# Performance work log

Measured on AMD Instinct MI355X. Metric: run time of the kernel, lower is better.

Reference implementation:

```python
import jax, jax.numpy as jnp
import numpy as np

C = 512
IC = C // 2
BN_EPS = 1e-5

def conv1x1(x, w, b):
    # x: (b,c,h,w), w: (o,c), b: (o,)
    return jnp.einsum('bchw,oc->bohw', x, w) + b[None, :, None, None]

def setup_inputs() -> dict:
    key = jax.random.key(0)
    ks = jax.random.split(key, 9)
    b, h, w = 8, 48, 48
    x = jax.random.normal(ks[0], (b, C, h, w), dtype=jnp.float32)
    s = 1.0 / np.sqrt(C)
    g_w = jax.random.normal(ks[1], (IC, C), dtype=jnp.float32) * s
    g_b = jnp.zeros((IC,), jnp.float32)
    theta_w = jax.random.normal(ks[2], (IC, C), dtype=jnp.float32) * s
    theta_b = jnp.zeros((IC,), jnp.float32)
    phi_w = jax.random.normal(ks[3], (IC, C), dtype=jnp.float32) * s
    phi_b = jnp.zeros((IC,), jnp.float32)
    w_w = jax.random.normal(ks[4], (C, IC), dtype=jnp.float32) * (1.0 / np.sqrt(IC))
    w_b = jnp.zeros((C,), jnp.float32)
    # BatchNorm affine params: initialized to 0 per nn.init.constant_ in source
    bn_gamma = jnp.zeros((C,), jnp.float32)
    bn_beta = jnp.zeros((C,), jnp.float32)
    return {"x": x, "g_w": g_w, "g_b": g_b, "theta_w": theta_w, "theta_b": theta_b,
            "phi_w": phi_w, "phi_b": phi_b, "w_w": w_w, "w_b": w_b,
            "bn_gamma": bn_gamma, "bn_beta": bn_beta}

def reference(x, g_w, g_b, theta_w, theta_b, phi_w, phi_b, w_w, w_b, bn_gamma, bn_beta):
    b, c, h, w = x.shape
    hw = h * w
    g_x = conv1x1(x, g_w, g_b).reshape(b, IC, hw).transpose(0, 2, 1)      # (b,hw,ic)
    theta_x = conv1x1(x, theta_w, theta_b).reshape(b, IC, hw).transpose(0, 2, 1)  # (b,hw,ic)
    phi_x = conv1x1(x, phi_w, phi_b).reshape(b, IC, hw)                    # (b,ic,hw)
    f = jnp.einsum('bqc,bck->bqk', theta_x, phi_x)                         # (b,hw,hw), unscaled
    f_div_C = jax.nn.softmax(f, axis=-1)
    y = jnp.einsum('bqk,bkc->bqc', f_div_C, g_x)                           # (b,hw,ic)
    y = y.transpose(0, 2, 1).reshape(b, IC, h, w)
    wy = conv1x1(y, w_w, w_b)                                              # (b,c,h,w)
    # BatchNorm2d in training mode: batch statistics over (b,h,w)
    mean = jnp.mean(wy, axis=(0, 2, 3), keepdims=True)
    var = jnp.var(wy, axis=(0, 2, 3), keepdims=True)
    wy_bn = (wy - mean) / jnp.sqrt(var + BN_EPS)
    wy_bn = wy_bn * bn_gamma[None, :, None, None] + bn_beta[None, :, None, None]
    return wy_bn + x
```

## Files before the change

kernel.cpp:

```cpp
#include <hip/hip_runtime.h>
#include <hip/hip_bf16.h>
#include <stdint.h>

constexpr int Bn  = 8;
constexpr int Cc  = 512;
constexpr int ICc = 256;
constexpr int HWc = 48 * 48;
constexpr float BN_EPS = 1e-5f;

typedef unsigned short u16;
typedef __attribute__((ext_vector_type(8))) short short8;
typedef __attribute__((ext_vector_type(4))) float f32x4;

__device__ __forceinline__ u16 f2bf(float f) {
    uint32_t u = __builtin_bit_cast(uint32_t, f);
    u += 0x7fffu + ((u >> 16) & 1u);
    return (u16)(u >> 16);
}
__device__ __forceinline__ void load_lds16(const void* g, void* l) {
    __builtin_amdgcn_global_load_lds(
        (const __attribute__((address_space(1))) void*)(uintptr_t)g,
        (__attribute__((address_space(3))) void*)(uintptr_t)l, 16, 0, 0);
}

__global__ __launch_bounds__(256)
void cast_front(const float* __restrict__ th_w, const float* __restrict__ ph_w,
                const float* __restrict__ g_w, const float* __restrict__ th_b,
                const float* __restrict__ ph_b, u16* __restrict__ wcat,
                float* __restrict__ bias_thph) {
    int idx = blockIdx.x * 256 + threadIdx.x;
    if (idx < 98304) {
        const float4* src;
        if (idx < 32768)       src = (const float4*)th_w + idx;
        else if (idx < 65536)  src = (const float4*)ph_w + (idx - 32768);
        else                   src = (const float4*)g_w  + (idx - 65536);
        float4 v = *src;
        ushort4 o;
        o.x = f2bf(v.x); o.y = f2bf(v.y); o.z = f2bf(v.z); o.w = f2bf(v.w);
        ((ushort4*)wcat)[idx] = o;
    } else if (idx < 98816) {
        int i = idx - 98304;
        bias_thph[i] = (i < 256) ? th_b[i] : ph_b[i - 256];
    }
}

__global__ __launch_bounds__(256)
void cast_w(const float* __restrict__ a, u16* __restrict__ out) {
    int idx = blockIdx.x * 256 + threadIdx.x;
    float4 v = ((const float4*)a)[idx];
    ushort4 o;
    o.x = f2bf(v.x); o.y = f2bf(v.y); o.z = f2bf(v.z); o.w = f2bf(v.w);
    ((ushort4*)out)[idx] = o;
}

__global__ __launch_bounds__(256)
void transpose_cast_x(const float* __restrict__ x, u16* __restrict__ xt) {
    __shared__ float t[64][33];
    const int b = blockIdx.z;
    const int p0 = blockIdx.x * 32;
    const int c0 = blockIdx.y * 64;
    const int tx = threadIdx.x & 31, ty = threadIdx.x >> 5;
    const float* xb = x + (size_t)b * Cc * HWc;
#pragma unroll
    for (int r = 0; r < 8; ++r)
        t[r * 8 + ty][tx] = xb[(size_t)(c0 + r * 8 + ty) * HWc + p0 + tx];
    __syncthreads();
    u16* xtb = xt + (size_t)b * HWc * Cc;
    const int cc = (threadIdx.x & 31) * 2, pp = threadIdx.x >> 5;
#pragma unroll
    for (int r = 0; r < 4; ++r) {
        int p = r * 8 + pp;
        ushort2 v;
        v.x = f2bf(t[cc][p]);
        v.y = f2bf(t[cc + 1][p]);
        *(ushort2*)&xtb[(size_t)(p0 + p) * Cc + c0 + cc] = v;
    }
}

template <int TM, int STORE, bool STATS>
__global__ __launch_bounds__(256, 2)
void mfma_gemm(const u16* __restrict__ A, const u16* __restrict__ B,
               void* __restrict__ Cout, const float* __restrict__ bias,
               int bias_mode, int K, int ldA, int ldB, int ldC,
               size_t sA, size_t sB, size_t sC,
               float* __restrict__ s0g, float* __restrict__ s1g) {
    constexpr int MI = TM / 32;
    __shared__ __align__(16) u16 As[TM * 32];
    __shared__ __align__(16) u16 Bs[128 * 32];
    const int bz = blockIdx.z;
    const int m0 = blockIdx.y * TM, n0 = blockIdx.x * 128;
    const u16* Ab = A + (size_t)bz * sA + (size_t)m0 * ldA;
    const u16* Bb = B + (size_t)bz * sB + (size_t)n0 * ldB;
    const int tid = threadIdx.x, lane = tid & 63, w = tid >> 6;
    const int wm = (w & 1) * (TM / 2);
    const int wn = (w >> 1) * 64;
    const int quad = lane >> 4, m16 = lane & 15;

    f32x4 acc[MI][4];
#pragma unroll
    for (int i = 0; i < MI; ++i)
#pragma unroll
        for (int j = 0; j < 4; ++j) acc[i][j] = (f32x4){0.f, 0.f, 0.f, 0.f};

    const int L0 = 2 * w * 64 + lane, L1 = L0 + 64;
    const int br0 = L0 >> 2, bc0 = (L0 & 3) * 8;
    const int br1 = L1 >> 2, bc1 = (L1 & 3) * 8;
    const int ar0 = (TM == 128) ? br0 : (tid >> 2);
    const int ac0 = (TM == 128) ? bc0 : (tid & 3) * 8;

    for (int k0 = 0; k0 < K; k0 += 32) {
        if (TM == 128) {
            load_lds16(Ab + (size_t)ar0 * ldA + k0 + ac0, &As[2 * w * 512]);
            load_lds16(Ab + (size_t)br1 * ldA + k0 + bc1, &As[(2 * w + 1) * 512]);
        } else {
            load_lds16(Ab + (size_t)ar0 * ldA + k0 + ac0, &As[w * 512]);
        }
        load_lds16(Bb + (size_t)br0 * ldB + k0 + bc0, &Bs[2 * w * 512]);
        load_lds16(Bb + (size_t)br1 * ldB + k0 + bc1, &Bs[(2 * w + 1) * 512]);
        __syncthreads();

        short8 af[MI], bfv[4];
#pragma unroll
        for (int i = 0; i < MI; ++i)
            af[i] = *(const short8*)&As[(wm + i * 16 + m16) * 32 + quad * 8];
#pragma unroll
        for (int j = 0; j < 4; ++j)
            bfv[j] = *(const short8*)&Bs[(wn + j * 16 + m16) * 32 + quad * 8];
#pragma unroll
        for (int i = 0; i < MI; ++i)
#pragma unroll
            for (int j = 0; j < 4; ++j)
                acc[i][j] = __builtin_amdgcn_mfma_f32_16x16x32_bf16(
                    af[i], bfv[j], acc[i][j], 0, 0, 0);
        __syncthreads();
    }

    if (bias_mode) {
#pragma unroll
        for (int i = 0; i < MI; ++i)
#pragma unroll
            for (int j = 0; j < 4; ++j)
#pragma unroll
                for (int r = 0; r < 4; ++r)
                    acc[i][j][r] += (bias_mode == 2)
                        ? bias[m0 + wm + i * 16 + quad * 4 + r]
                        : bias[n0 + wn + j * 16 + m16];
    }

    if (STORE == 0) {
        u16* C = (u16*)Cout + (size_t)bz * sC;
#pragma unroll
        for (int i = 0; i < MI; ++i) {
            int m = m0 + wm + i * 16 + quad * 4;
#pragma unroll
            for (int j = 0; j < 4; ++j) {
                int n = n0 + wn + j * 16 + m16;
#pragma unroll
                for (int r = 0; r < 4; ++r)
                    C[(size_t)(m + r) * ldC + n] = f2bf(acc[i][j][r]);
            }
        }
    } else {
        float* C = (float*)Cout + (size_t)bz * sC;
#pragma unroll
        for (int i = 0; i < MI; ++i) {
            int m = m0 + wm + i * 16 + quad * 4;
#pragma unroll
            for (int j = 0; j < 4; ++j) {
                int n = n0 + wn + j * 16 + m16;
#pragma unroll
                for (int r = 0; r < 4; ++r)
                    C[(size_t)(m + r) * ldC + n] = acc[i][j][r];
            }
        }
    }

    if (STATS) {
#pragma unroll
        for (int i = 0; i < MI; ++i) {
#pragma unroll
            for (int r = 0; r < 4; ++r) {
                float v0 = 0.f, v1 = 0.f;
#pragma unroll
                for (int j = 0; j < 4; ++j) {
                    float v = acc[i][j][r];
                    v0 += v;
                    v1 = fmaf(v, v, v1);
                }
#pragma unroll
                for (int off = 8; off; off >>= 1) {
                    v0 += __shfl_down(v0, off, 16);
                    v1 += __shfl_down(v1, off, 16);
                }
                if (m16 == 0) {
                    int m = m0 + wm + i * 16 + quad * 4 + r;
                    atomicAdd(&s0g[m], v0);
                    atomicAdd(&s1g[m], v1);
                }
            }
        }
    }
}

__global__ __launch_bounds__(256, 2)
void flash_attn(const u16* __restrict__ thph, const u16* __restrict__ g,
                u16* __restrict__ y) {
    __shared__ __align__(16) u16 smem[25088];
    const int bz = blockIdx.y;
    const int q0 = blockIdx.x * 64;
    const u16* Qb = thph + (size_t)bz * HWc * 512 + (size_t)q0 * 512;
    const u16* Kb = thph + (size_t)bz * HWc * 512 + 256;
    const u16* Vb = g + (size_t)bz * ICc * HWc;
    const int tid = threadIdx.x, lane = tid & 63, w = tid >> 6;
    const int quad = lane >> 4, m16 = lane & 15;
    const int wm = w * 16;

#pragma unroll
    for (int t = 0; t < 8; ++t) {
        int L = (w * 8 + t) * 64 + lane;
        int row = L >> 5, col = (L & 31) * 8;
        load_lds16(Qb + (size_t)row * 512 + col, &smem[8192 + (w * 8 + t) * 512]);
    }
    __syncthreads();
    short8 qf[8];
#pragma unroll
    for (int c = 0; c < 8; ++c)
        qf[c] = *(const short8*)&smem[8192 + (wm + m16) * 256 + c * 32 + quad * 8];
    __syncthreads();

    f32x4 O[16];
#pragma unroll
    for (int i = 0; i < 16; ++i) O[i] = (f32x4){0.f, 0.f, 0.f, 0.f};
    float mrow[4] = {-1e30f, -1e30f, -1e30f, -1e30f};
    float lrow[4] = {0.f, 0.f, 0.f, 0.f};

    for (int kt = 0; kt < 18; ++kt) {
        const u16* Kt = Kb + (size_t)kt * 128 * 512;
        f32x4 Sa[8];
#pragma unroll
        for (int j = 0; j < 8; ++j) Sa[j] = (f32x4){0.f, 0.f, 0.f, 0.f};

#pragma unroll
        for (int kc = 0; kc < 4; ++kc) {
#pragma unroll
            for (int h = 0; h < 2; ++h) {
                int cdim = (kc * 2 + h) * 32;
#pragma unroll
                for (int t = 0; t < 2; ++t) {
                    int L = (w * 2 + t) * 64 + lane;
                    int row = L >> 2, col = (L & 3) * 8;
                    load_lds16(Kt + (size_t)row * 512 + cdim + col,
                               &smem[h * 4096 + (w * 2 + t) * 512]);
                }
            }
            __syncthreads();
#pragma unroll
            for (int h = 0; h < 2; ++h)
#pragma unroll
                for (int j = 0; j < 8; ++j) {
                    short8 kf = *(const short8*)
                        &smem[h * 4096 + (j * 16 + m16) * 32 + quad * 8];
                    Sa[j] = __builtin_amdgcn_mfma_f32_16x16x32_bf16(
                        qf[kc * 2 + h], kf, Sa[j], 0, 0, 0);
                }
            __syncthreads();
        }

        float alpha[4];
#pragma unroll
        for (int r = 0; r < 4; ++r) {
            float tm = Sa[0][r];
#pragma unroll
            for (int j = 1; j < 8; ++j) tm = fmaxf(tm, Sa[j][r]);
#pragma unroll
            for (int off = 1; off < 16; off <<= 1)
                tm = fmaxf(tm, __shfl_xor(tm, off, 16));
            float nm = fmaxf(mrow[r], tm);
            alpha[r] = __expf(mrow[r] - nm);
            mrow[r] = nm;
            float ps = 0.f;
#pragma unroll
            for (int j = 0; j < 8; ++j) {
                float p = __expf(Sa[j][r] - nm);
                Sa[j][r] = p;
                ps += p;
            }
#pragma unroll
            for (int off = 1; off < 16; off <<= 1)
                ps += __shfl_xor(ps, off, 16);
            lrow[r] = lrow[r] * alpha[r] + ps;
        }
#pragma unroll
        for (int j2 = 0; j2 < 16; ++j2)
#pragma unroll
            for (int r = 0; r < 4; ++r) O[j2][r] *= alpha[r];

        u16* Pw = &smem[16384 + w * 2176];
#pragma unroll
        for (int j = 0; j < 8; ++j)
#pragma unroll
            for (int r = 0; r < 4; ++r)
                Pw[(quad * 4 + r) * 136 + j * 16 + m16] = f2bf(Sa[j][r]);
        short8 pf[4];
#pragma unroll
        for (int c2 = 0; c2 < 4; ++c2)
            pf[c2] = *(const short8*)&Pw[m16 * 136 + c2 * 32 + quad * 8];

#pragma unroll
        for (int c2 = 0; c2 < 4; ++c2) {
            int keyc = kt * 128 + c2 * 32;
#pragma unroll
            for (int t = 0; t < 4; ++t) {
                int L = (w * 4 + t) * 64 + lane;
                int row = L >> 2, col = (L & 3) * 8;
                load_lds16(Vb + (size_t)row * HWc + keyc + col,
                           &smem[8192 + (w * 4 + t) * 512]);
            }
            __syncthreads();
#pragma unroll
            for (int j2 = 0; j2 < 16; ++j2) {
                short8 vf = *(const short8*)
                    &smem[8192 + (j2 * 16 + m16) * 32 + quad * 8];
                O[j2] = __builtin_amdgcn_mfma_f32_16x16x32_bf16(
                    pf[c2], vf, O[j2], 0, 0, 0);
            }
            __syncthreads();
        }
    }

    float rinv[4];
#pragma unroll
    for (int r = 0; r < 4; ++r) rinv[r] = 1.0f / lrow[r];
    u16* yb = y + ((size_t)bz * HWc + q0 + wm) * ICc;
#pragma unroll
    for (int j2 = 0; j2 < 16; ++j2)
#pragma unroll
        for (int r = 0; r < 4; ++r)
            yb[(size_t)(quad * 4 + r) * ICc + j2 * 16 + m16] =
                f2bf(O[j2][r] * rinv[r]);
}

__global__ __launch_bounds__(256)
void bn_apply(const float* __restrict__ wy, const float* __restrict__ x,
              const float* __restrict__ s0, const float* __restrict__ s1,
              const float* __restrict__ gamma, const float* __restrict__ beta,
              float* __restrict__ out) {
    const size_t i4 = (size_t)blockIdx.x * 256 + threadIdx.x;
    const size_t base = i4 * 4;
    const int o = (int)((base / HWc) % Cc);
    const float N = (float)(Bn * HWc);
    const float mean = s0[o] / N;
    const float var  = s1[o] / N - mean * mean;
    const float rstd = rsqrtf(var + BN_EPS);
    const float ga = gamma[o];
    const float be = beta[o];
    const float4 w4 = ((const float4*)wy)[i4];
    const float4 x4 = ((const float4*)x)[i4];
    float4 r;
    r.x = (w4.x - mean) * rstd * ga + be + x4.x;
    r.y = (w4.y - mean) * rstd * ga + be + x4.y;
    r.z = (w4.z - mean) * rstd * ga + be + x4.z;
    r.w = (w4.w - mean) * rstd * ga + be + x4.w;
    ((float4*)out)[i4] = r;
}

extern "C" void kernel_launch(void* const* d_in, const int* in_sizes, int n_in,
                              void* d_out, int out_size, void* d_ws, size_t ws_size,
                              hipStream_t stream) {
    const float* x     = (const float*)d_in[0];
    const float* g_w   = (const float*)d_in[1];
    const float* g_b   = (const float*)d_in[2];
    const float* th_w  = (const float*)d_in[3];
    const float* th_b  = (const float*)d_in[4];
    const float* ph_w  = (const float*)d_in[5];
    const float* ph_b  = (const float*)d_in[6];
    const float* w_w   = (const float*)d_in[7];
    const float* w_b   = (const float*)d_in[8];
    const float* gamma = (const float*)d_in[9];
    const float* beta  = (const float*)d_in[10];

    char* base = (char*)d_ws;
    u16* thph = (u16*)base;
    u16* g    = (u16*)(base + 18874368);
    u16* xt   = (u16*)(base + 28311552);
    u16* wcat = (u16*)(base + 47185920);
    float* bias_thph = (float*)(base + 47972352);
    u16* wbf2 = (u16*)(base + 47974400);
    float* stats = (float*)(base + 48236544);
    u16* y    = (u16*)(base + 48240640);
    float* wy = (float*)(base + 57677824);

    dim3 blk(256);
    const u16* thphw = wcat;
    const u16* gwb   = wcat + 262144;

    cast_front<<<dim3(386), blk, 0, stream>>>(th_w, ph_w, g_w, th_b, ph_b,
                                              wcat, bias_thph);
    cast_w<<<dim3(128), blk, 0, stream>>>(w_w, wbf2);
    hipMemsetAsync(stats, 0, 2 * Cc * sizeof(float), stream);
    transpose_cast_x<<<dim3(HWc / 32, Cc / 64, Bn), blk, 0, stream>>>(x, xt);

    mfma_gemm<128, 0, false><<<dim3(4, 18, Bn), blk, 0, stream>>>(
        xt, thphw, thph, bias_thph, 1, Cc, Cc, Cc, 512,
        (size_t)HWc * Cc, 0, (size_t)HWc * 512, nullptr, nullptr);

    mfma_gemm<64, 0, false><<<dim3(18, 4, Bn), blk, 0, stream>>>(
        gwb, xt, g, g_b, 2, Cc, Cc, Cc, HWc,
        0, (size_t)HWc * Cc, (size_t)ICc * HWc, nullptr, nullptr);

    flash_attn<<<dim3(HWc / 64, Bn), blk, 0, stream>>>(thph, g, y);

    mfma_gemm<128, 1, true><<<dim3(18, 4, Bn), blk, 0, stream>>>(
        wbf2, y, wy, w_b, 2, ICc, ICc, ICc, HWc,
        0, (size_t)HWc * ICc, (size_t)Cc * HWc, stats, stats + Cc);

    bn_apply<<<dim3((Bn * Cc * HWc) / 4 / 256), blk, 0, stream>>>(
        wy, x, stats, stats + Cc, gamma, beta, (float*)d_out);
}
```

Measured before the change: 361.1 us.

## Split flash attention over key range with partial outputs and combine kernel

Result: slower. 391.0 us (+8.3%).

```diff
diff --git a/kernel.cpp b/kernel.cpp
--- a/kernel.cpp
+++ b/kernel.cpp
@@ -7,6 +7,9 @@
 constexpr int ICc = 256;
 constexpr int HWc = 48 * 48;
 constexpr float BN_EPS = 1e-5f;
+constexpr int NSPLIT = 3;
+constexpr int KSP = HWc / NSPLIT;
+constexpr int NKT = KSP / 64;
 
 typedef unsigned short u16;
 typedef __attribute__((ext_vector_type(8))) short short8;
@@ -202,31 +205,34 @@
     }
 }
 
-__global__ __launch_bounds__(256, 2)
+__global__ __launch_bounds__(256, 3)
 void flash_attn(const u16* __restrict__ thph, const u16* __restrict__ g,
-                u16* __restrict__ y) {
-    __shared__ __align__(16) u16 smem[25088];
-    const int bz = blockIdx.y;
+                float* __restrict__ Opart, float* __restrict__ mpart,
+                float* __restrict__ lpart) {
+    __shared__ __align__(16) u16 smem[16384 + 4 * 1088];
+    const int bz = blockIdx.z, split = blockIdx.y;
     const int q0 = blockIdx.x * 64;
+    const int ks = split * KSP;
     const u16* Qb = thph + (size_t)bz * HWc * 512 + (size_t)q0 * 512;
     const u16* Kb = thph + (size_t)bz * HWc * 512 + 256;
     const u16* Vb = g + (size_t)bz * ICc * HWc;
     const int tid = threadIdx.x, lane = tid & 63, w = tid >> 6;
     const int quad = lane >> 4, m16 = lane & 15;
     const int wm = w * 16;
-
-#pragma unroll
-    for (int t = 0; t < 8; ++t) {
-        int L = (w * 8 + t) * 64 + lane;
-        int row = L >> 5, col = (L & 31) * 8;
-        load_lds16(Qb + (size_t)row * 512 + col, &smem[8192 + (w * 8 + t) * 512]);
+    u16* Pw = &smem[16384 + w * 1088];
+
+#pragma unroll
+    for (int it = 0; it < 8; ++it) {
+        int L = it * 256 + tid;
+        int c = L >> 8, s = L & 255;
+        load_lds16(Qb + (size_t)(s >> 2) * 512 + c * 32 + (s & 3) * 8,
+                   &smem[(it * 256 + w * 64) * 8]);
     }
     __syncthreads();
     short8 qf[8];
 #pragma unroll
     for (int c = 0; c < 8; ++c)
-        qf[c] = *(const short8*)&smem[8192 + (wm + m16) * 256 + c * 32 + quad * 8];
-    __syncthreads();
+        qf[c] = *(const short8*)&smem[c * 2048 + (wm + m16) * 32 + quad * 8];
 
     f32x4 O[16];
 #pragma unroll
@@ -234,44 +240,37 @@
     float mrow[4] = {-1e30f, -1e30f, -1e30f, -1e30f};
     float lrow[4] = {0.f, 0.f, 0.f, 0.f};
 
-    for (int kt = 0; kt < 18; ++kt) {
-        const u16* Kt = Kb + (size_t)kt * 128 * 512;
-        f32x4 Sa[8];
-#pragma unroll
-        for (int j = 0; j < 8; ++j) Sa[j] = (f32x4){0.f, 0.f, 0.f, 0.f};
-
-#pragma unroll
-        for (int kc = 0; kc < 4; ++kc) {
-#pragma unroll
-            for (int h = 0; h < 2; ++h) {
-                int cdim = (kc * 2 + h) * 32;
-#pragma unroll
-                for (int t = 0; t < 2; ++t) {
-                    int L = (w * 2 + t) * 64 + lane;
-                    int row = L >> 2, col = (L & 3) * 8;
-                    load_lds16(Kt + (size_t)row * 512 + cdim + col,
-                               &smem[h * 4096 + (w * 2 + t) * 512]);
-                }
-            }
-            __syncthreads();
-#pragma unroll
-            for (int h = 0; h < 2; ++h)
-#pragma unroll
-                for (int j = 0; j < 8; ++j) {
-                    short8 kf = *(const short8*)
-                        &smem[h * 4096 + (j * 16 + m16) * 32 + quad * 8];
-                    Sa[j] = __builtin_amdgcn_mfma_f32_16x16x32_bf16(
-                        qf[kc * 2 + h], kf, Sa[j], 0, 0, 0);
-                }
-            __syncthreads();
-        }
+    for (int kt = 0; kt < NKT; ++kt) {
+        const u16* Kt = Kb + (size_t)(ks + kt * 64) * 512;
+        __syncthreads();
+#pragma unroll
+        for (int it = 0; it < 8; ++it) {
+            int L = it * 256 + tid;
+            int c = L >> 8, s = L & 255;
+            load_lds16(Kt + (size_t)(s >> 2) * 512 + c * 32 + (s & 3) * 8,
+                       &smem[(it * 256 + w * 64) * 8]);
+        }
+        __syncthreads();
+
+        f32x4 Sa[4];
+#pragma unroll
+        for (int j = 0; j < 4; ++j) Sa[j] = (f32x4){0.f, 0.f, 0.f, 0.f};
+#pragma unroll
+        for (int kc = 0; kc < 8; ++kc)
+#pragma unroll
+            for (int j = 0; j < 4; ++j) {
+                short8 kf = *(const short8*)
+                    &smem[kc * 2048 + (j * 16 + m16) * 32 + quad * 8];
+                Sa[j] = __builtin_amdgcn_mfma_f32_16x16x32_bf16(
+                    qf[kc], kf, Sa[j], 0, 0, 0);
+            }
 
         float alpha[4];
 #pragma unroll
         for (int r = 0; r < 4; ++r) {
             float tm = Sa[0][r];
 #pragma unroll
-            for (int j = 1; j < 8; ++j) tm = fmaxf(tm, Sa[j][r]);
+            for (int j = 1; j < 4; ++j) tm = fmaxf(tm, Sa[j][r]);
 #pragma unroll
             for (int off = 1; off < 16; off <<= 1)
                 tm = fmaxf(tm, __shfl_xor(tm, off, 16));
@@ -280,7 +279,7 @@
             mrow[r] = nm;
             float ps = 0.f;
 #pragma unroll
-            for (int j = 0; j < 8; ++j) {
+            for (int j = 0; j < 4; ++j) {
                 float p = __expf(Sa[j][r] - nm);
                 Sa[j][r] = p;
                 ps += p;
@@ -295,49 +294,80 @@
 #pragma unroll
             for (int r = 0; r < 4; ++r) O[j2][r] *= alpha[r];
 
-        u16* Pw = &smem[16384 + w * 2176];
-#pragma unroll
-        for (int j = 0; j < 8; ++j)
+#pragma unroll
+        for (int j = 0; j < 4; ++j)
 #pragma unroll
             for (int r = 0; r < 4; ++r)
-                Pw[(quad * 4 + r) * 136 + j * 16 + m16] = f2bf(Sa[j][r]);
-        short8 pf[4];
-#pragma unroll
-        for (int c2 = 0; c2 < 4; ++c2)
-            pf[c2] = *(const short8*)&Pw[m16 * 136 + c2 * 32 + quad * 8];
-
-#pragma unroll
-        for (int c2 = 0; c2 < 4; ++c2) {
-            int keyc = kt * 128 + c2 * 32;
-#pragma unroll
-            for (int t = 0; t < 4; ++t) {
-                int L = (w * 4 + t) * 64 + lane;
-                int row = L >> 2, col = (L & 3) * 8;
-                load_lds16(Vb + (size_t)row * HWc + keyc + col,
-                           &smem[8192 + (w * 4 + t) * 512]);
-            }
-            __syncthreads();
+                Pw[(j >> 1) * 512 + (quad * 4 + r) * 32 + (j & 1) * 16 + m16] =
+                    f2bf(Sa[j][r]);
+        short8 pf[2];
+#pragma unroll
+        for (int c2 = 0; c2 < 2; ++c2)
+            pf[c2] = *(const short8*)&Pw[c2 * 512 + m16 * 32 + quad * 8];
+
+        __syncthreads();
+        const u16* Vt = Vb + ks + kt * 64;
+#pragma unroll
+        for (int it = 0; it < 8; ++it) {
+            int L = it * 256 + tid;
+            int c2 = L >> 10, s = L & 1023;
+            load_lds16(Vt + (size_t)(s >> 2) * HWc + c2 * 32 + (s & 3) * 8,
+                       &smem[(it * 256 + w * 64) * 8]);
+        }
+        __syncthreads();
+
+#pragma unroll
+        for (int c2 = 0; c2 < 2; ++c2)
 #pragma unroll
             for (int j2 = 0; j2 < 16; ++j2) {
                 short8 vf = *(const short8*)
-                    &smem[8192 + (j2 * 16 + m16) * 32 + quad * 8];
+                    &smem[c2 * 8192 + (j2 * 16 + m16) * 32 + quad * 8];
                 O[j2] = __builtin_amdgcn_mfma_f32_16x16x32_bf16(
                     pf[c2], vf, O[j2], 0, 0, 0);
             }
-            __syncthreads();
-        }
-    }
-
-    float rinv[4];
-#pragma unroll
-    for (int r = 0; r < 4; ++r) rinv[r] = 1.0f / lrow[r];
-    u16* yb = y + ((size_t)bz * HWc + q0 + wm) * ICc;
+    }
+
+    float* Ob = Opart + ((size_t)(split * Bn + bz) * HWc + q0 + wm) * ICc;
 #pragma unroll
     for (int j2 = 0; j2 < 16; ++j2)
 #pragma unroll
         for (int r = 0; r < 4; ++r)
-            yb[(size_t)(quad * 4 + r) * ICc + j2 * 16 + m16] =
-                f2bf(O[j2][r] * rinv[r]);
+            Ob[(size_t)(quad * 4 + r) * ICc + j2 * 16 + m16] = O[j2][r];
+    if (m16 == 0) {
+#pragma unroll
+        for (int r = 0; r < 4; ++r) {
+            size_t idx = (size_t)(split * Bn + bz) * HWc + q0 + wm + quad * 4 + r;
+            mpart[idx] = mrow[r];
+            lpart[idx] = lrow[r];
+        }
+    }
+}
+
+__global__ __launch_bounds__(256)
+void flash_combine(const float* __restrict__ Opart, const float* __restrict__ mpart,
+                   const float* __restrict__ lpart, u16* __restrict__ y) {
+    const int b = blockIdx.y;
+    const int q = blockIdx.x * 4 + (threadIdx.x >> 6);
+    const int ic = (threadIdx.x & 63) * 4;
+    const size_t rq = (size_t)b * HWc + q;
+    const size_t SS = (size_t)Bn * HWc;
+
+    float m0 = mpart[rq], m1 = mpart[SS + rq], m2 = mpart[2 * SS + rq];
+    float M = fmaxf(m0, fmaxf(m1, m2));
+    float w0 = __expf(m0 - M), w1 = __expf(m1 - M), w2 = __expf(m2 - M);
+    float L = lpart[rq] * w0 + lpart[SS + rq] * w1 + lpart[2 * SS + rq] * w2;
+    float inv = 1.0f / L;
+    w0 *= inv; w1 *= inv; w2 *= inv;
+
+    f32x4 o0 = *(const f32x4*)&Opart[rq * ICc + ic];
+    f32x4 o1 = *(const f32x4*)&Opart[(SS + rq) * ICc + ic];
+    f32x4 o2 = *(const f32x4*)&Opart[(2 * SS + rq) * ICc + ic];
+    ushort4 o;
+    o.x = f2bf(o0[0] * w0 + o1[0] * w1 + o2[0] * w2);
+    o.y = f2bf(o0[1] * w0 + o1[1] * w1 + o2[1] * w2);
+    o.z = f2bf(o0[2] * w0 + o1[2] * w1 + o2[2] * w2);
+    o.w = f2bf(o0[3] * w0 + o1[3] * w1 + o2[3] * w2);
+    *(ushort4*)&y[rq * ICc + ic] = o;
 }
 
 __global__ __launch_bounds__(256)
@@ -382,13 +412,17 @@
     char* base = (char*)d_ws;
     u16* thph = (u16*)base;
     u16* g    = (u16*)(base + 18874368);
-    u16* xt   = (u16*)(base + 28311552);
-    u16* wcat = (u16*)(base + 47185920);
-    float* bias_thph = (float*)(base + 47972352);
-    u16* wbf2 = (u16*)(base + 47974400);
-    float* stats = (float*)(base + 48236544);
-    u16* y    = (u16*)(base + 48240640);
-    float* wy = (float*)(base + 57677824);
+    u16* y    = (u16*)(base + 28311552);
+    u16* wbf2 = (u16*)(base + 37748736);
+    float* stats = (float*)(base + 38010880);
+    float* bias_thph = (float*)(base + 38014976);
+    u16* wcat = (u16*)(base + 38017024);
+    char* R   = base + 38803456;
+    u16* xt   = (u16*)R;
+    float* Opart = (float*)R;
+    float* mpart = (float*)(R + 56623104);
+    float* lpart = (float*)(R + 56844288);
+    float* wy = (float*)R;
 
     dim3 blk(256);
     const u16* thphw = wcat;
@@ -408,7 +442,9 @@
         gwb, xt, g, g_b, 2, Cc, Cc, Cc, HWc,
         0, (size_t)HWc * Cc, (size_t)ICc * HWc, nullptr, nullptr);
 
-    flash_attn<<<dim3(HWc / 64, Bn), blk, 0, stream>>>(thph, g, y);
+    flash_attn<<<dim3(HWc / 64, NSPLIT, Bn), blk, 0, stream>>>(
+        thph, g, Opart, mpart, lpart);
+    flash_combine<<<dim3(HWc / 4, Bn), blk, 0, stream>>>(Opart, mpart, lpart, y);
 
     mfma_gemm<128, 1, true><<<dim3(18, 4, Bn), blk, 0, stream>>>(
         wbf2, y, wy, w_b, 2, ICc, ICc, ICc, HWc,
```
